# Kernel tuning notes

Measured on AMD Instinct MI355X. Metric: run time of the kernel, lower is better.

The kernel has to match this reference:

```python
import jax, jax.numpy as jnp
import numpy as np

T, B, IN_DIM, D_VALUE, D_KEY = 1024, 8, 512, 64, 64
EPS = 1e-8

def setup_inputs() -> dict:
    key = jax.random.key(0)
    ks = jax.random.split(key, 7)
    s = 1.0 / np.sqrt(IN_DIM)
    return {
        "x":  jax.random.normal(ks[0], (T, B, IN_DIM), dtype=jnp.float32),
        "Wv": jax.random.uniform(ks[1], (D_VALUE, IN_DIM), jnp.float32, -s, s),
        "bv": jax.random.uniform(ks[2], (D_VALUE,), jnp.float32, -s, s),
        "Wk": jax.random.uniform(ks[3], (D_KEY, IN_DIM), jnp.float32, -s, s),
        "bk": jax.random.uniform(ks[4], (D_KEY,), jnp.float32, -s, s),
        "Wa": jax.random.uniform(ks[5], (D_KEY, IN_DIM), jnp.float32, -s, s),
        "ba": jax.random.uniform(ks[6], (D_KEY,), jnp.float32, -s, s),
    }

def reference(x, Wv, bv, Wk, bk, Wa, ba):
    # Projections: x (T,B,in_dim) -> v (T,B,d), k (T,B,n), alpha (T,B,n)
    v = jnp.einsum('tbi,di->tbd', x, Wv) + bv
    k = jnp.einsum('tbi,ni->tbn', x, Wk) + bk
    alpha = jax.nn.sigmoid(jnp.einsum('tbi,ni->tbn', x, Wa) + ba)
    # outer product per timestep: (T,B,d,n)
    outer = jnp.einsum('tbd,tbn->tbdn', v, k)
    # log-space cumulative decay, normalized by final cumprod
    log_cumprod = jnp.cumsum(jnp.log(jnp.maximum(alpha, EPS)), axis=0)  # (T,B,n)
    cumprod = jnp.exp(log_cumprod)
    decay = cumprod / (cumprod[-1:] + EPS)
    weighted = outer * decay[:, :, None, :]  # (T,B,d,n)
    S = jnp.cumsum(weighted, axis=0)
    return S
```

## Files before the change

### kernel.cpp

```cpp
#include <hip/hip_runtime.h>
#include <math.h>

#define T_DIM  1024
#define B_DIM  8
#define IN_D   512
#define NROWS  (T_DIM * B_DIM)
#define EPSF   1e-8f

#define CHUNK  32
#define NCHUNK (T_DIM / CHUNK)
#define SEG    64
#define NSEG   (T_DIM / SEG)

typedef float vfloat4 __attribute__((ext_vector_type(4)));

#define OFF_WT   0
#define OFF_V    (OFF_WT + IN_D * 192)
#define OFF_K    (OFF_V  + NROWS * 64)
#define OFF_Z    (OFF_K  + NROWS * 64)
#define OFF_SEG  (OFF_Z  + NROWS * 64)
#define OFF_TOT  (OFF_SEG + NSEG * B_DIM * 64)
#define OFF_P    (OFF_TOT + B_DIM * 64)

__global__ void k0_wt(const float* __restrict__ Wv, const float* __restrict__ Wk,
                      const float* __restrict__ Wa, float* __restrict__ Wt) {
    int idx = blockIdx.x * 256 + threadIdx.x;
    int i = idx / 192, c = idx % 192;
    float v;
    if (c < 64)       v = Wv[c * IN_D + i];
    else if (c < 128) v = Wk[(c - 64) * IN_D + i];
    else              v = Wa[(c - 128) * IN_D + i];
    Wt[i * 192 + c] = v;
}

__global__ __launch_bounds__(512) void k1_proj(
        const float* __restrict__ x, const float* __restrict__ Wt,
        const float* __restrict__ bv, const float* __restrict__ bk, const float* __restrict__ ba,
        float* __restrict__ V, float* __restrict__ Kb, float* __restrict__ Zb) {
    __shared__ float xs[32 * 64];
    __shared__ float wsm[64 * 192];
    const int tid = threadIdx.x;
    const int c  = tid & 63;
    const int rg = tid >> 6;
    const int row0 = blockIdx.x * 32;

    float acc[4][3];
#pragma unroll
    for (int j = 0; j < 4; ++j) { acc[j][0] = 0.f; acc[j][1] = 0.f; acc[j][2] = 0.f; }

    for (int ks = 0; ks < IN_D; ks += 64) {
        {
            int r = tid >> 4, f = tid & 15;
            float4 v4 = reinterpret_cast<const float4*>(x)[((row0 + r) * IN_D + ks) / 4 + f];
            reinterpret_cast<float4*>(xs)[r * 16 + f] = v4;
        }
#pragma unroll
        for (int q = 0; q < 6; ++q) {
            int i = tid + q * 512;
            int kk = i / 48, f = i % 48;
            float4 v4 = reinterpret_cast<const float4*>(Wt)[((ks + kk) * 192) / 4 + f];
            reinterpret_cast<float4*>(wsm)[kk * 48 + f] = v4;
        }
        __syncthreads();

        for (int kk = 0; kk < 64; kk += 4) {
            float4 xv[4];
#pragma unroll
            for (int j = 0; j < 4; ++j)
                xv[j] = reinterpret_cast<const float4*>(xs)[((rg + 8 * j) * 64 + kk) >> 2];
#pragma unroll
            for (int q = 0; q < 4; ++q) {
                float w0 = wsm[(kk + q) * 192 + c];
                float w1 = wsm[(kk + q) * 192 + 64 + c];
                float w2 = wsm[(kk + q) * 192 + 128 + c];
#pragma unroll
                for (int j = 0; j < 4; ++j) {
                    float xx = (&xv[j].x)[q];
                    acc[j][0] = fmaf(xx, w0, acc[j][0]);
                    acc[j][1] = fmaf(xx, w1, acc[j][1]);
                    acc[j][2] = fmaf(xx, w2, acc[j][2]);
                }
            }
        }
        __syncthreads();
    }
    float bvc = bv[c], bkc = bk[c], bac = ba[c];
#pragma unroll
    for (int j = 0; j < 4; ++j) {
        int row = row0 + rg + 8 * j;
        V[row * 64 + c]  = acc[j][0] + bvc;
        Kb[row * 64 + c] = acc[j][1] + bkc;
        Zb[row * 64 + c] = acc[j][2] + bac;
    }
}

__global__ void k2a_logs(float* __restrict__ Z, float* __restrict__ seg) {
    int b = blockIdx.x & 7, s = blockIdx.x >> 3;
    int n = threadIdx.x;
    int base = b * 64 + n;
    float accv = 0.f;
    for (int i = 0; i < SEG; ++i) {
        int t = s * SEG + i;
        float z = Z[t * 512 + base];
        float a = 1.f / (1.f + expf(-z));
        float l = logf(fmaxf(a, EPSF));
        Z[t * 512 + base] = l;
        accv += l;
    }
    seg[s * 512 + base] = accv;
}

__global__ void k2b_scan(float* __restrict__ seg, float* __restrict__ tot) {
    int i = threadIdx.x;
    float run = 0.f;
#pragma unroll
    for (int s = 0; s < NSEG; ++s) {
        float v = seg[s * 512 + i];
        seg[s * 512 + i] = run;
        run += v;
    }
    tot[i] = run;
}

__global__ void k2c_w(const float* __restrict__ Z, const float* __restrict__ seg,
                      const float* __restrict__ tot, float* __restrict__ Kb) {
    int b = blockIdx.x & 7, s = blockIdx.x >> 3;
    int n = threadIdx.x;
    int base = b * 64 + n;
    float run = seg[s * 512 + base];
    float invden = 1.f / (expf(tot[base]) + EPSF);
    for (int i = 0; i < SEG; ++i) {
        int t = s * SEG + i;
        run += Z[t * 512 + base];
        float decay = expf(run) * invden;
        Kb[t * 512 + base] *= decay;
    }
}

__global__ __launch_bounds__(256) void k3_partial(const float* __restrict__ V,
                                                  const float* __restrict__ W,
                                                  float* __restrict__ P) {
    __shared__ float vs[CHUNK * 64];
    __shared__ float wsh[CHUNK * 64];
    int b = blockIdx.x & 7, cch = blockIdx.x >> 3;
    int tid = threadIdx.x;
    int dg = tid >> 4, n4 = tid & 15;
#pragma unroll
    for (int q = 0; q < 2; ++q) {
        int i = tid + q * 256;
        int il = i >> 4, f = i & 15;
        int row = (cch * CHUNK + il) * 8 + b;
        reinterpret_cast<float4*>(vs)[il * 16 + f]  = reinterpret_cast<const float4*>(V)[row * 16 + f];
        reinterpret_cast<float4*>(wsh)[il * 16 + f] = reinterpret_cast<const float4*>(W)[row * 16 + f];
    }
    __syncthreads();
    float4 acc[4];
#pragma unroll
    for (int q = 0; q < 4; ++q) acc[q] = make_float4(0.f, 0.f, 0.f, 0.f);

#pragma unroll 4
    for (int i = 0; i < CHUNK; ++i) {
        float4 wv = reinterpret_cast<const float4*>(wsh)[i * 16 + n4];
#pragma unroll
        for (int q = 0; q < 4; ++q) {
            float vd = vs[i * 64 + dg + 16 * q];
            acc[q].x = fmaf(vd, wv.x, acc[q].x);
            acc[q].y = fmaf(vd, wv.y, acc[q].y);
            acc[q].z = fmaf(vd, wv.z, acc[q].z);
            acc[q].w = fmaf(vd, wv.w, acc[q].w);
        }
    }
    float* Pp = P + (cch * 8 + b) * 4096;
#pragma unroll
    for (int q = 0; q < 4; ++q)
        *reinterpret_cast<float4*>(Pp + (dg + 16 * q) * 64 + 4 * n4) = acc[q];
}

__global__ void k4_prefix(float* __restrict__ P) {
    int gid = blockIdx.x * 256 + threadIdx.x;
    int b = gid >> 12, dn = gid & 4095;
    float vals[NCHUNK];
#pragma unroll
    for (int c = 0; c < NCHUNK; ++c) vals[c] = P[(c * 8 + b) * 4096 + dn];
    float run = 0.f;
#pragma unroll
    for (int c = 0; c < NCHUNK; ++c) { P[(c * 8 + b) * 4096 + dn] = run; run += vals[c]; }
}

__global__ __launch_bounds__(256) void k5_main(const float* __restrict__ V,
                                               const float* __restrict__ W,
                                               const float* __restrict__ P,
                                               float* __restrict__ S) {
    __shared__ float vs[CHUNK * 64];
    __shared__ float wsh[CHUNK * 64];
    int b = blockIdx.x & 7, cch = blockIdx.x >> 3;
    int tid = threadIdx.x;
    int dg = tid >> 4, n4 = tid & 15;
#pragma unroll
    for (int q = 0; q < 2; ++q) {
        int i = tid + q * 256;
        int il = i >> 4, f = i & 15;
        int row = (cch * CHUNK + il) * 8 + b;
        reinterpret_cast<float4*>(vs)[il * 16 + f]  = reinterpret_cast<const float4*>(V)[row * 16 + f];
        reinterpret_cast<float4*>(wsh)[il * 16 + f] = reinterpret_cast<const float4*>(W)[row * 16 + f];
    }
    vfloat4 acc[4];
    const float* Pp = P + (cch * 8 + b) * 4096;
#pragma unroll
    for (int q = 0; q < 4; ++q)
        acc[q] = *reinterpret_cast<const vfloat4*>(Pp + (dg + 16 * q) * 64 + 4 * n4);
    __syncthreads();

#pragma unroll 4
    for (int i = 0; i < CHUNK; ++i) {
        float4 wv = reinterpret_cast<const float4*>(wsh)[i * 16 + n4];
        int t = cch * CHUNK + i;
        float* Sb = S + (size_t)t * 32768 + b * 4096;
#pragma unroll
        for (int q = 0; q < 4; ++q) {
            float vd = vs[i * 64 + dg + 16 * q];
            acc[q].x = fmaf(vd, wv.x, acc[q].x);
            acc[q].y = fmaf(vd, wv.y, acc[q].y);
            acc[q].z = fmaf(vd, wv.z, acc[q].z);
            acc[q].w = fmaf(vd, wv.w, acc[q].w);
            __builtin_nontemporal_store(acc[q],
                reinterpret_cast<vfloat4*>(Sb + (dg + 16 * q) * 64 + 4 * n4));
        }
    }
}

extern "C" void kernel_launch(void* const* d_in, const int* in_sizes, int n_in,
                              void* d_out, int out_size, void* d_ws, size_t ws_size,
                              hipStream_t stream) {
    const float* x  = (const float*)d_in[0];
    const float* Wv = (const float*)d_in[1];
    const float* bv = (const float*)d_in[2];
    const float* Wk = (const float*)d_in[3];
    const float* bk = (const float*)d_in[4];
    const float* Wa = (const float*)d_in[5];
    const float* ba = (const float*)d_in[6];
    float* S  = (float*)d_out;
    float* ws = (float*)d_ws;

    float* Wt  = ws + OFF_WT;
    float* V   = ws + OFF_V;
    float* Kb  = ws + OFF_K;
    float* Zb  = ws + OFF_Z;
    float* seg = ws + OFF_SEG;
    float* tot = ws + OFF_TOT;
    float* P   = ws + OFF_P;

    k0_wt     <<<384, 256, 0, stream>>>(Wv, Wk, Wa, Wt);
    k1_proj   <<<256, 512, 0, stream>>>(x, Wt, bv, bk, ba, V, Kb, Zb);
    k2a_logs  <<<128,  64, 0, stream>>>(Zb, seg);
    k2b_scan  <<<  1, 512, 0, stream>>>(seg, tot);
    k2c_w     <<<128,  64, 0, stream>>>(Zb, seg, tot, Kb);
    k3_partial<<<256, 256, 0, stream>>>(V, Kb, P);
    k4_prefix <<<128, 256, 0, stream>>>(P);
    k5_main   <<<256, 256, 0, stream>>>(V, Kb, P, S);
}
```

Before: 233.3 us.

## Rework projection GEMM with split-K register tiling and shrink scan chunk sizes

The projection kernel is rewritten to use 256 threads. Each thread computes a 4x4x3 register tile, the K dimension is split into two halves across thread groups, and the halves are combined through shared memory. The scan chunk and segment sizes are cut from 32/64 to 16, which raises block counts in the log, decay, partial and main kernels, and several loops are fully unrolled. The aim is more parallelism in the short serial scan stages and more data reuse per thread in the GEMM. The cost is a larger chunk prefix (64 chunks) and a redundant dead computation in the reduction epilogue.

```diff
diff --git a/kernel.cpp b/kernel.cpp
--- a/kernel.cpp
+++ b/kernel.cpp
@@ -7,9 +7,9 @@
 #define NROWS  (T_DIM * B_DIM)
 #define EPSF   1e-8f
 
-#define CHUNK  32
+#define CHUNK  16
 #define NCHUNK (T_DIM / CHUNK)
-#define SEG    64
+#define SEG    16
 #define NSEG   (T_DIM / SEG)
 
 typedef float vfloat4 __attribute__((ext_vector_type(4)));
@@ -33,64 +33,103 @@
     Wt[i * 192 + c] = v;
 }
 
-__global__ __launch_bounds__(512) void k1_proj(
+__global__ __launch_bounds__(256) void k1_proj(
         const float* __restrict__ x, const float* __restrict__ Wt,
         const float* __restrict__ bv, const float* __restrict__ bk, const float* __restrict__ ba,
         float* __restrict__ V, float* __restrict__ Kb, float* __restrict__ Zb) {
-    __shared__ float xs[32 * 64];
-    __shared__ float wsm[64 * 192];
-    const int tid = threadIdx.x;
-    const int c  = tid & 63;
-    const int rg = tid >> 6;
+    __shared__ float xs[2][32][32];
+    __shared__ float wsm[2][32][192];
+    const int tid  = threadIdx.x;
+    const int h    = tid >> 7;
+    const int t7   = tid & 127;
+    const int rq   = t7 >> 4;
+    const int cq   = t7 & 15;
     const int row0 = blockIdx.x * 32;
 
-    float acc[4][3];
-#pragma unroll
-    for (int j = 0; j < 4; ++j) { acc[j][0] = 0.f; acc[j][1] = 0.f; acc[j][2] = 0.f; }
-
-    for (int ks = 0; ks < IN_D; ks += 64) {
-        {
-            int r = tid >> 4, f = tid & 15;
-            float4 v4 = reinterpret_cast<const float4*>(x)[((row0 + r) * IN_D + ks) / 4 + f];
-            reinterpret_cast<float4*>(xs)[r * 16 + f] = v4;
-        }
-#pragma unroll
-        for (int q = 0; q < 6; ++q) {
-            int i = tid + q * 512;
-            int kk = i / 48, f = i % 48;
-            float4 v4 = reinterpret_cast<const float4*>(Wt)[((ks + kk) * 192) / 4 + f];
-            reinterpret_cast<float4*>(wsm)[kk * 48 + f] = v4;
+    float4 acc[4][3];
+#pragma unroll
+    for (int j = 0; j < 4; ++j)
+#pragma unroll
+        for (int m = 0; m < 3; ++m) acc[j][m] = make_float4(0.f, 0.f, 0.f, 0.f);
+
+    for (int s = 0; s < 8; ++s) {
+#pragma unroll
+        for (int q = 0; q < 2; ++q) {
+            int idx = tid + q * 256;
+            int hh = idx >> 8, r = idx & 31, f = (idx >> 5) & 7;
+            float4 v4 = reinterpret_cast<const float4*>(x)[((row0 + r) * IN_D + hh * 256 + s * 32 + f * 4) >> 2];
+            xs[hh][f * 4 + 0][r] = v4.x;
+            xs[hh][f * 4 + 1][r] = v4.y;
+            xs[hh][f * 4 + 2][r] = v4.z;
+            xs[hh][f * 4 + 3][r] = v4.w;
+        }
+#pragma unroll
+        for (int q = 0; q < 12; ++q) {
+            int idx = tid + q * 256;
+            int hh = idx / 1536;
+            int rem = idx - hh * 1536;
+            int kk = rem / 48;
+            int f  = rem - kk * 48;
+            float4 v4 = reinterpret_cast<const float4*>(Wt)[((hh * 256 + s * 32 + kk) * 192 + f * 4) >> 2];
+            *reinterpret_cast<float4*>(&wsm[hh][kk][f * 4]) = v4;
         }
         __syncthreads();
 
-        for (int kk = 0; kk < 64; kk += 4) {
-            float4 xv[4];
-#pragma unroll
-            for (int j = 0; j < 4; ++j)
-                xv[j] = reinterpret_cast<const float4*>(xs)[((rg + 8 * j) * 64 + kk) >> 2];
-#pragma unroll
-            for (int q = 0; q < 4; ++q) {
-                float w0 = wsm[(kk + q) * 192 + c];
-                float w1 = wsm[(kk + q) * 192 + 64 + c];
-                float w2 = wsm[(kk + q) * 192 + 128 + c];
+#pragma unroll 4
+        for (int kk = 0; kk < 32; ++kk) {
+            float4 xv = *reinterpret_cast<const float4*>(&xs[h][kk][rq * 4]);
+#pragma unroll
+            for (int m = 0; m < 3; ++m) {
+                float4 wq = *reinterpret_cast<const float4*>(&wsm[h][kk][m * 64 + cq * 4]);
 #pragma unroll
                 for (int j = 0; j < 4; ++j) {
-                    float xx = (&xv[j].x)[q];
-                    acc[j][0] = fmaf(xx, w0, acc[j][0]);
-                    acc[j][1] = fmaf(xx, w1, acc[j][1]);
-                    acc[j][2] = fmaf(xx, w2, acc[j][2]);
+                    float xx = (&xv.x)[j];
+                    acc[j][m].x = fmaf(xx, wq.x, acc[j][m].x);
+                    acc[j][m].y = fmaf(xx, wq.y, acc[j][m].y);
+                    acc[j][m].z = fmaf(xx, wq.z, acc[j][m].z);
+                    acc[j][m].w = fmaf(xx, wq.w, acc[j][m].w);
                 }
             }
         }
         __syncthreads();
     }
-    float bvc = bv[c], bkc = bk[c], bac = ba[c];
-#pragma unroll
-    for (int j = 0; j < 4; ++j) {
-        int row = row0 + rg + 8 * j;
-        V[row * 64 + c]  = acc[j][0] + bvc;
-        Kb[row * 64 + c] = acc[j][1] + bkc;
-        Zb[row * 64 + c] = acc[j][2] + bac;
+
+    float* red = &wsm[0][0][0];
+    if (h == 1) {
+#pragma unroll
+        for (int j = 0; j < 4; ++j)
+#pragma unroll
+            for (int m = 0; m < 3; ++m)
+                *reinterpret_cast<float4*>(&red[t7 * 52 + (j * 3 + m) * 4]) = acc[j][m];
+    }
+    __syncthreads();
+    if (h == 0) {
+        float4 bv4 = *reinterpret_cast<const float4*>(&bv[cq * 4]);
+        float4 bk4 = *reinterpret_cast<const float4*>(&bk[cq * 4]);
+        float4 ba4 = *reinterpret_cast<const float4*>(&ba[cq * 4]);
+#pragma unroll
+        for (int j = 0; j < 4; ++j) {
+            int row = row0 + rq * 4 + j;
+#pragma unroll
+            for (int m = 0; m < 3; ++m) {
+                float4 o = *reinterpret_cast<const float4*>(&red[t7 * 52 + (j * 3 + m) * 4]);
+                o.x += (&acc[j][m].x)[0];
+                o.x = acc[j][m].x + (&o.x)[0] - acc[j][m].x;
+            }
+            float4 o0 = *reinterpret_cast<const float4*>(&red[t7 * 52 + (j * 3 + 0) * 4]);
+            float4 o1 = *reinterpret_cast<const float4*>(&red[t7 * 52 + (j * 3 + 1) * 4]);
+            float4 o2 = *reinterpret_cast<const float4*>(&red[t7 * 52 + (j * 3 + 2) * 4]);
+            float4 r0, r1, r2;
+            r0.x = acc[j][0].x + o0.x + bv4.x; r0.y = acc[j][0].y + o0.y + bv4.y;
+            r0.z = acc[j][0].z + o0.z + bv4.z; r0.w = acc[j][0].w + o0.w + bv4.w;
+            r1.x = acc[j][1].x + o1.x + bk4.x; r1.y = acc[j][1].y + o1.y + bk4.y;
+            r1.z = acc[j][1].z + o1.z + bk4.z; r1.w = acc[j][1].w + o1.w + bk4.w;
+            r2.x = acc[j][2].x + o2.x + ba4.x; r2.y = acc[j][2].y + o2.y + ba4.y;
+            r2.z = acc[j][2].z + o2.z + ba4.z; r2.w = acc[j][2].w + o2.w + ba4.w;
+            *reinterpret_cast<float4*>(&V [row * 64 + cq * 4]) = r0;
+            *reinterpret_cast<float4*>(&Kb[row * 64 + cq * 4]) = r1;
+            *reinterpret_cast<float4*>(&Zb[row * 64 + cq * 4]) = r2;
+        }
     }
 }
 
@@ -99,6 +138,7 @@
     int n = threadIdx.x;
     int base = b * 64 + n;
     float accv = 0.f;
+#pragma unroll
     for (int i = 0; i < SEG; ++i) {
         int t = s * SEG + i;
         float z = Z[t * 512 + base];
@@ -112,13 +152,12 @@
 
 __global__ void k2b_scan(float* __restrict__ seg, float* __restrict__ tot) {
     int i = threadIdx.x;
+    float vals[NSEG];
+#pragma unroll
+    for (int s = 0; s < NSEG; ++s) vals[s] = seg[s * 512 + i];
     float run = 0.f;
 #pragma unroll
-    for (int s = 0; s < NSEG; ++s) {
-        float v = seg[s * 512 + i];
-        seg[s * 512 + i] = run;
-        run += v;
-    }
+    for (int s = 0; s < NSEG; ++s) { seg[s * 512 + i] = run; run += vals[s]; }
     tot[i] = run;
 }
 
@@ -129,11 +168,11 @@
     int base = b * 64 + n;
     float run = seg[s * 512 + base];
     float invden = 1.f / (expf(tot[base]) + EPSF);
+#pragma unroll
     for (int i = 0; i < SEG; ++i) {
         int t = s * SEG + i;
         run += Z[t * 512 + base];
-        float decay = expf(run) * invden;
-        Kb[t * 512 + base] *= decay;
+        Kb[t * 512 + base] *= expf(run) * invden;
     }
 }
 
@@ -145,10 +184,8 @@
     int b = blockIdx.x & 7, cch = blockIdx.x >> 3;
     int tid = threadIdx.x;
     int dg = tid >> 4, n4 = tid & 15;
-#pragma unroll
-    for (int q = 0; q < 2; ++q) {
-        int i = tid + q * 256;
-        int il = i >> 4, f = i & 15;
+    {
+        int il = tid >> 4, f = tid & 15;
         int row = (cch * CHUNK + il) * 8 + b;
         reinterpret_cast<float4*>(vs)[il * 16 + f]  = reinterpret_cast<const float4*>(V)[row * 16 + f];
         reinterpret_cast<float4*>(wsh)[il * 16 + f] = reinterpret_cast<const float4*>(W)[row * 16 + f];
@@ -158,7 +195,7 @@
 #pragma unroll
     for (int q = 0; q < 4; ++q) acc[q] = make_float4(0.f, 0.f, 0.f, 0.f);
 
-#pragma unroll 4
+#pragma unroll
     for (int i = 0; i < CHUNK; ++i) {
         float4 wv = reinterpret_cast<const float4*>(wsh)[i * 16 + n4];
 #pragma unroll
@@ -176,15 +213,16 @@
         *reinterpret_cast<float4*>(Pp + (dg + 16 * q) * 64 + 4 * n4) = acc[q];
 }
 
-__global__ void k4_prefix(float* __restrict__ P) {
+__global__ __launch_bounds__(256) void k4_prefix(float* __restrict__ P) {
     int gid = blockIdx.x * 256 + threadIdx.x;
     int b = gid >> 12, dn = gid & 4095;
-    float vals[NCHUNK];
-#pragma unroll
-    for (int c = 0; c < NCHUNK; ++c) vals[c] = P[(c * 8 + b) * 4096 + dn];
     float run = 0.f;
 #pragma unroll
-    for (int c = 0; c < NCHUNK; ++c) { P[(c * 8 + b) * 4096 + dn] = run; run += vals[c]; }
+    for (int c = 0; c < NCHUNK; ++c) {
+        float v = P[(c * 8 + b) * 4096 + dn];
+        P[(c * 8 + b) * 4096 + dn] = run;
+        run += v;
+    }
 }
 
 __global__ __launch_bounds__(256) void k5_main(const float* __restrict__ V,
@@ -196,10 +234,8 @@
     int b = blockIdx.x & 7, cch = blockIdx.x >> 3;
     int tid = threadIdx.x;
     int dg = tid >> 4, n4 = tid & 15;
-#pragma unroll
-    for (int q = 0; q < 2; ++q) {
-        int i = tid + q * 256;
-        int il = i >> 4, f = i & 15;
+    {
+        int il = tid >> 4, f = tid & 15;
         int row = (cch * CHUNK + il) * 8 + b;
         reinterpret_cast<float4*>(vs)[il * 16 + f]  = reinterpret_cast<const float4*>(V)[row * 16 + f];
         reinterpret_cast<float4*>(wsh)[il * 16 + f] = reinterpret_cast<const float4*>(W)[row * 16 + f];
@@ -211,7 +247,7 @@
         acc[q] = *reinterpret_cast<const vfloat4*>(Pp + (dg + 16 * q) * 64 + 4 * n4);
     __syncthreads();
 
-#pragma unroll 4
+#pragma unroll
     for (int i = 0; i < CHUNK; ++i) {
         float4 wv = reinterpret_cast<const float4*>(wsh)[i * 16 + n4];
         int t = cch * CHUNK + i;
@@ -251,11 +287,11 @@
     float* P   = ws + OFF_P;
 
     k0_wt     <<<384, 256, 0, stream>>>(Wv, Wk, Wa, Wt);
-    k1_proj   <<<256, 512, 0, stream>>>(x, Wt, bv, bk, ba, V, Kb, Zb);
-    k2a_logs  <<<128,  64, 0, stream>>>(Zb, seg);
+    k1_proj   <<<256, 256, 0, stream>>>(x, Wt, bv, bk, ba, V, Kb, Zb);
+    k2a_logs  <<<512,  64, 0, stream>>>(Zb, seg);
     k2b_scan  <<<  1, 512, 0, stream>>>(seg, tot);
-    k2c_w     <<<128,  64, 0, stream>>>(Zb, seg, tot, Kb);
-    k3_partial<<<256, 256, 0, stream>>>(V, Kb, P);
+    k2c_w     <<<512,  64, 0, stream>>>(Zb, seg, tot, Kb);
+    k3_partial<<<512, 256, 0, stream>>>(V, Kb, P);
     k4_prefix <<<128, 256, 0, stream>>>(P);
-    k5_main   <<<256, 256, 0, stream>>>(V, Kb, P, S);
-}
+    k5_main   <<<512, 256, 0, stream>>>(V, Kb, P, S);
+}
```

After: 212.7 us. -8.8%, faster.
